# Performance work log

Measured on AMD Instinct MI355X. Metric: run time of the kernel, lower is better.

The kernel has to match this reference:

```python
import jax, jax.numpy as jnp
import numpy as np

D_MODEL = 1024
NUM_HEADS = 16
D_K = D_MODEL // NUM_HEADS
D_FF = 4096
LN_EPS = 1e-5


def layernorm(x, gamma, beta):
    mu = jnp.mean(x, axis=-1, keepdims=True)
    var = jnp.mean(jnp.square(x - mu), axis=-1, keepdims=True)
    return (x - mu) * jax.lax.rsqrt(var + LN_EPS) * gamma + beta


def setup_inputs() -> dict:
    key = jax.random.key(0)
    ks = jax.random.split(key, 16)
    s = 1.0 / np.sqrt(D_MODEL)
    sf = 1.0 / np.sqrt(D_FF)
    inp = {
        "x": jax.random.normal(ks[0], (2, 2048, D_MODEL), dtype=jnp.float32),
        # attention sublayer LN
        "ln1_g": jnp.ones((D_MODEL,), jnp.float32),
        "ln1_b": jnp.zeros((D_MODEL,), jnp.float32),
        # QKV / output projections, stored as [in, out]
        "Wq": jax.random.uniform(ks[1], (D_MODEL, D_MODEL), jnp.float32, -s, s),
        "bq": jax.random.uniform(ks[2], (D_MODEL,), jnp.float32, -s, s),
        "Wk": jax.random.uniform(ks[3], (D_MODEL, D_MODEL), jnp.float32, -s, s),
        "bk": jax.random.uniform(ks[4], (D_MODEL,), jnp.float32, -s, s),
        "Wv": jax.random.uniform(ks[5], (D_MODEL, D_MODEL), jnp.float32, -s, s),
        "bv": jax.random.uniform(ks[6], (D_MODEL,), jnp.float32, -s, s),
        "Wo": jax.random.uniform(ks[7], (D_MODEL, D_MODEL), jnp.float32, -s, s),
        "bo": jax.random.uniform(ks[8], (D_MODEL,), jnp.float32, -s, s),
        # FFN sublayer LN
        "ln2_g": jnp.ones((D_MODEL,), jnp.float32),
        "ln2_b": jnp.zeros((D_MODEL,), jnp.float32),
        "W1": jax.random.uniform(ks[9], (D_MODEL, D_FF), jnp.float32, -s, s),
        "b1": jax.random.uniform(ks[10], (D_FF,), jnp.float32, -s, s),
        "W2": jax.random.uniform(ks[11], (D_FF, D_MODEL), jnp.float32, -sf, sf),
        "b2": jax.random.uniform(ks[12], (D_MODEL,), jnp.float32, -sf, sf),
    }
    return inp


def block_fwd(x, ln1_g, ln1_b, Wq, bq, Wk, bk, Wv, bv, Wo, bo,
              ln2_g, ln2_b, W1, b1, W2, b2):
    B, S, D = x.shape
    # --- attention sublayer (pre-LN + residual) ---
    h = layernorm(x, ln1_g, ln1_b)
    q = (h @ Wq + bq).reshape(B, S, NUM_HEADS, D_K)
    k = (h @ Wk + bk).reshape(B, S, NUM_HEADS, D_K)
    v = (h @ Wv + bv).reshape(B, S, NUM_HEADS, D_K)
    scale = 1.0 / np.sqrt(D_K)  # == sqrt(d_k)/d_k in source
    attn = jnp.einsum("bqhd,bkhd->bhqk", q, k) * scale  # [B,H,S,S]
    causal = jnp.arange(S)[:, None] >= jnp.arange(S)[None, :]
    attn = jnp.where(causal, attn, -jnp.inf)
    score = jax.nn.softmax(attn, axis=-1)
    o = jnp.einsum("bhqk,bkhd->bqhd", score, v).reshape(B, S, D)
    x = x + (o @ Wo + bo)
    # --- FFN sublayer (pre-LN + residual) ---
    h = layernorm(x, ln2_g, ln2_b)
    h = jax.nn.gelu(h @ W1 + b1, approximate=False)  # torch nn.GELU = exact erf
    return x + (h @ W2 + b2)


def reference(x, ln1_g, ln1_b, Wq, bq, Wk, bk, Wv, bv, Wo, bo,
              ln2_g, ln2_b, W1, b1, W2, b2):
    return block_fwd(x, ln1_g, ln1_b, Wq, bq, Wk, bk, Wv, bv, Wo, bo,
                     ln2_g, ln2_b, W1, b1, W2, b2)
```

## Files before the change

### kernel.cpp

```cpp
#include <hip/hip_runtime.h>
#include <hip/hip_bf16.h>
#include <hip/hip_fp8.h>
#include <math.h>

typedef unsigned short u16;
typedef unsigned char u8;
typedef unsigned int u32;
typedef long i64;
typedef __bf16 bf16x8 __attribute__((ext_vector_type(8)));
typedef float f32x4 __attribute__((ext_vector_type(4)));

#define MFMA16(a, b, c) __builtin_amdgcn_mfma_f32_16x16x32_bf16(a, b, c, 0, 0, 0)
#define MFMA8(a, b, c) __builtin_amdgcn_mfma_f32_16x16x32_fp8_fp8(a, b, c, 0, 0, 0)

__device__ __forceinline__ u16 f2b(float f) {
    __bf16 h = (__bf16)f;
    return __builtin_bit_cast(u16, h);
}

__device__ __forceinline__ u8 f2f8(float f) {
    __hip_fp8_e4m3 h(f);
    return h.__x;
}

__device__ __forceinline__ void gld16(const void* g, void* l) {
    __builtin_amdgcn_global_load_lds(
        (const __attribute__((address_space(1))) unsigned int*)g,
        (__attribute__((address_space(3))) unsigned int*)l, 16, 0, 0);
}

__global__ __launch_bounds__(256) void transpose_all(
    const float* __restrict__ Wq, const float* __restrict__ Wk,
    const float* __restrict__ Wv, const float* __restrict__ Wo,
    const float* __restrict__ W1, const float* __restrict__ W2, u16* __restrict__ wqkvT,
    u16* __restrict__ woT, u16* __restrict__ w1T, u8* __restrict__ w2T8) {
    __shared__ float tile[32][33];
    int t = blockIdx.x;
    const float* in;
    u16* out = nullptr;
    int R, C;
    bool isf8 = false;
    if (t < 3072) {
        int m = t >> 10;
        t &= 1023;
        in = m == 0 ? Wq : (m == 1 ? Wk : Wv);
        out = wqkvT + m * 1048576;
        R = 1024; C = 1024;
    } else if (t < 4096) {
        t -= 3072; in = Wo; out = woT; R = 1024; C = 1024;
    } else if (t < 8192) {
        t -= 4096; in = W1; out = w1T; R = 1024; C = 4096;
    } else {
        t -= 8192; in = W2; R = 4096; C = 1024; isf8 = true;
    }
    int tilesX = C >> 5;
    int c0 = (t % tilesX) * 32, r0 = (t / tilesX) * 32;
    int tx = threadIdx.x, ty = threadIdx.y;
#pragma unroll
    for (int i = 0; i < 4; i++)
        tile[ty + i * 8][tx] = in[(size_t)(r0 + ty + i * 8) * C + c0 + tx];
    __syncthreads();
    if (isf8) {
#pragma unroll
        for (int i = 0; i < 4; i++)
            w2T8[(size_t)(c0 + ty + i * 8) * R + r0 + tx] = f2f8(tile[tx][ty + i * 8] * 64.0f);
    } else {
#pragma unroll
        for (int i = 0; i < 4; i++)
            out[(size_t)(c0 + ty + i * 8) * R + r0 + tx] = f2b(tile[tx][ty + i * 8]);
    }
}

__global__ __launch_bounds__(256) void ln_kernel(const float* __restrict__ x,
                                                 const float* __restrict__ g,
                                                 const float* __restrict__ b,
                                                 u16* __restrict__ out) {
    int row = blockIdx.x;
    int tid = threadIdx.x;
    const float* xr = x + (size_t)row * 1024;
    float4 v = ((const float4*)xr)[tid];
    float s = v.x + v.y + v.z + v.w;
    float s2 = v.x * v.x + v.y * v.y + v.z * v.z + v.w * v.w;
#pragma unroll
    for (int off = 32; off > 0; off >>= 1) {
        s += __shfl_xor(s, off);
        s2 += __shfl_xor(s2, off);
    }
    __shared__ float ps[4], ps2[4];
    int wid = tid >> 6;
    if ((tid & 63) == 0) { ps[wid] = s; ps2[wid] = s2; }
    __syncthreads();
    s = ps[0] + ps[1] + ps[2] + ps[3];
    s2 = ps2[0] + ps2[1] + ps2[2] + ps2[3];
    float mu = s * (1.0f / 1024.0f);
    float var = s2 * (1.0f / 1024.0f) - mu * mu;
    float rs = rsqrtf(var + 1e-5f);
    int c = tid * 4;
    ushort4 o;
    o.x = f2b((v.x - mu) * rs * g[c + 0] + b[c + 0]);
    o.y = f2b((v.y - mu) * rs * g[c + 1] + b[c + 1]);
    o.z = f2b((v.z - mu) * rs * g[c + 2] + b[c + 2]);
    o.w = f2b((v.w - mu) * rs * g[c + 3] + b[c + 3]);
    ((ushort4*)(out + (size_t)row * 1024))[tid] = o;
}

__global__ __launch_bounds__(256) void vtrans_kernel(const u16* __restrict__ Vb,
                                                     u16* __restrict__ VbT) {
    __shared__ u16 t[64][66];
    const int tid = threadIdx.x;
    const int s0 = blockIdx.x * 64;
    const int bh = blockIdx.y;
    const u16* src = Vb + (size_t)bh * 2048 * 64;
    u16* dst = VbT + (size_t)bh * 64 * 2048;
#pragma unroll
    for (int p = 0; p < 2; p++) {
        int idx = p * 256 + tid;
        int r = idx >> 3, dc = (idx & 7) * 8;
        uint4 v = *(const uint4*)&src[(size_t)(s0 + r) * 64 + dc];
        const u16* pv = (const u16*)&v;
#pragma unroll
        for (int j = 0; j < 8; j++) t[r][dc + j] = pv[j];
    }
    __syncthreads();
    int d = tid >> 2, sc = (tid & 3) * 16;
    u16 buf[16];
#pragma unroll
    for (int m = 0; m < 16; m++) {
        int cp = sc + m;
        int blk = cp >> 5, c = cp & 31;
        int srcw = blk * 32 + (c >> 1) + (c & 1) * 16;
        buf[m] = t[srcw][d];
    }
    *(uint4*)&dst[(size_t)d * 2048 + s0 + sc] = *(uint4*)&buf[0];
    *(uint4*)&dst[(size_t)d * 2048 + s0 + sc + 8] = *(uint4*)&buf[8];
}

#define EPI_QKV 0
#define EPI_RESID 1
#define EPI_GELU 2

__device__ __forceinline__ void gemm_stage(const u16* __restrict__ A,
                                           const u16* __restrict__ BT,
                                           u16 (&Asb)[128][32], u16 (&Bsb)[128][32],
                                           int m0, int n0, int K, int k0, int sr, int sdc,
                                           int wb) {
    gld16(&A[(size_t)(m0 + sr) * K + k0 + sdc], &Asb[0][0] + wb);
    gld16(&A[(size_t)(m0 + 64 + sr) * K + k0 + sdc], &Asb[0][0] + 2048 + wb);
    gld16(&BT[(size_t)(n0 + sr) * K + k0 + sdc], &Bsb[0][0] + wb);
    gld16(&BT[(size_t)(n0 + 64 + sr) * K + k0 + sdc], &Bsb[0][0] + 2048 + wb);
}

__device__ __forceinline__ void gemm_compute(const u16 (&Asb)[128][32],
                                             const u16 (&Bsb)[128][32], f32x4 (&acc)[4][4],
                                             int wm, int wn, int quad, int c15) {
    bf16x8 af[4], bfr[4];
#pragma unroll
    for (int i = 0; i < 4; i++) af[i] = *(const bf16x8*)&Asb[wm + i * 16 + c15][quad * 8];
#pragma unroll
    for (int j = 0; j < 4; j++) bfr[j] = *(const bf16x8*)&Bsb[wn + j * 16 + c15][quad * 8];
#pragma unroll
    for (int i = 0; i < 4; i++)
#pragma unroll
        for (int j = 0; j < 4; j++) acc[i][j] = MFMA16(af[i], bfr[j], acc[i][j]);
}

template <int EPI>
__global__ __launch_bounds__(256) void gemm_kernel(const u16* __restrict__ A,
                                                   const u16* __restrict__ BT,
                                                   const float* __restrict__ bias0,
                                                   const float* __restrict__ bias1,
                                                   const float* __restrict__ bias2,
                                                   void* __restrict__ outp,
                                                   const float* __restrict__ resid,
                                                   int N, int K) {
    __shared__ __align__(16) u16 As0[128][32], Bs0[128][32];
    __shared__ __align__(16) u16 As1[128][32], Bs1[128][32];
    const int tid = threadIdx.x;
    const int m0 = blockIdx.y * 128, n0 = blockIdx.x * 128;
    const int w = tid >> 6, lid = tid & 63, quad = lid >> 4, c15 = lid & 15;
    const int wm = (w >> 1) * 64, wn = (w & 1) * 64;
    const int sr = tid >> 2, sdc = (tid & 3) * 8;
    const int wb = (tid & 192) * 8;

    f32x4 acc[4][4] = {};

    gemm_stage(A, BT, As0, Bs0, m0, n0, K, 0, sr, sdc, wb);
    const int KT = K >> 5;
    for (int kt = 0; kt < KT; kt += 2) {
        __syncthreads();
        gemm_stage(A, BT, As1, Bs1, m0, n0, K, (kt + 1) << 5, sr, sdc, wb);
        gemm_compute(As0, Bs0, acc, wm, wn, quad, c15);
        __syncthreads();
        if (kt + 2 < KT) gemm_stage(A, BT, As0, Bs0, m0, n0, K, (kt + 2) << 5, sr, sdc, wb);
        gemm_compute(As1, Bs1, acc, wm, wn, quad, c15);
    }

    const int which = n0 >> 10;
    const float* bias = (EPI == EPI_QKV) ? (which == 0 ? bias0 : (which == 1 ? bias1 : bias2))
                                         : bias0;
    u16* qkv_dst = (u16*)outp + (size_t)which * 4194304;

#pragma unroll
    for (int i = 0; i < 4; i++) {
#pragma unroll
        for (int j = 0; j < 4; j++) {
#pragma unroll
            for (int r = 0; r < 4; r++) {
                int gr = m0 + wm + i * 16 + quad * 4 + r;
                int gc = n0 + wn + j * 16 + c15;
                if (EPI == EPI_QKV) {
                    int lc = gc & 1023;
                    float v = acc[i][j][r] + bias[lc];
                    int bb = gr >> 11, ss = gr & 2047, hh = lc >> 6, dd = lc & 63;
                    qkv_dst[((size_t)((bb * 16 + hh) * 2048 + ss)) * 64 + dd] = f2b(v);
                } else if (EPI == EPI_RESID) {
                    float v = acc[i][j][r] + bias[gc];
                    ((float*)outp)[(size_t)gr * N + gc] = resid[(size_t)gr * N + gc] + v;
                } else {
                    float v = acc[i][j][r] + bias[gc];
                    float u = v * (0.79788456f + 0.03567741f * v * v);
                    float e = __expf(2.0f * u);
                    float th = 1.0f - 2.0f / (e + 1.0f);
                    ((u8*)outp)[(size_t)gr * N + gc] = f2f8(0.5f * v * (1.0f + th));
                }
            }
        }
    }
}

__device__ __forceinline__ void gemm8_stage(const u8* __restrict__ A,
                                            const u8* __restrict__ BT, u8 (&Asb)[128][32],
                                            u8 (&Bsb)[128][32], int m0, int n0, int K,
                                            int k0, int sr, int sdc, int wbB) {
    gld16(&A[(size_t)(m0 + sr) * K + k0 + sdc], &Asb[0][0] + wbB);
    gld16(&BT[(size_t)(n0 + sr) * K + k0 + sdc], &Bsb[0][0] + wbB);
}

__device__ __forceinline__ void gemm8_compute(const u8 (&Asb)[128][32],
                                              const u8 (&Bsb)[128][32], f32x4 (&acc)[4][4],
                                              int wm, int wn, int quad, int c15) {
    i64 af[4], bfr[4];
#pragma unroll
    for (int i = 0; i < 4; i++) af[i] = *(const i64*)&Asb[wm + i * 16 + c15][quad * 8];
#pragma unroll
    for (int j = 0; j < 4; j++) bfr[j] = *(const i64*)&Bsb[wn + j * 16 + c15][quad * 8];
#pragma unroll
    for (int i = 0; i < 4; i++)
#pragma unroll
        for (int j = 0; j < 4; j++) acc[i][j] = MFMA8(af[i], bfr[j], acc[i][j]);
}

__global__ __launch_bounds__(256) void gemm_fp8_kernel(const u8* __restrict__ A,
                                                       const u8* __restrict__ BT,
                                                       const float* __restrict__ bias,
                                                       float* __restrict__ outp,
                                                       const float* __restrict__ resid,
                                                       int N, int K) {
    __shared__ __align__(16) u8 As0[128][32], Bs0[128][32];
    __shared__ __align__(16) u8 As1[128][32], Bs1[128][32];
    const int tid = threadIdx.x;
    const int m0 = blockIdx.y * 128, n0 = blockIdx.x * 128;
    const int w = tid >> 6, lid = tid & 63, quad = lid >> 4, c15 = lid & 15;
    const int wm = (w >> 1) * 64, wn = (w & 1) * 64;
    const int sr = tid >> 1, sdc = (tid & 1) * 16;
    const int wbB = (tid & 192) * 16;

    f32x4 acc[4][4] = {};

    gemm8_stage(A, BT, As0, Bs0, m0, n0, K, 0, sr, sdc, wbB);
    const int KT = K >> 5;
    for (int kt = 0; kt < KT; kt += 2) {
        __syncthreads();
        gemm8_stage(A, BT, As1, Bs1, m0, n0, K, (kt + 1) << 5, sr, sdc, wbB);
        gemm8_compute(As0, Bs0, acc, wm, wn, quad, c15);
        __syncthreads();
        if (kt + 2 < KT) gemm8_stage(A, BT, As0, Bs0, m0, n0, K, (kt + 2) << 5, sr, sdc, wbB);
        gemm8_compute(As1, Bs1, acc, wm, wn, quad, c15);
    }

#pragma unroll
    for (int i = 0; i < 4; i++) {
#pragma unroll
        for (int j = 0; j < 4; j++) {
#pragma unroll
            for (int r = 0; r < 4; r++) {
                int gr = m0 + wm + i * 16 + quad * 4 + r;
                int gc = n0 + wn + j * 16 + c15;
                float v = acc[i][j][r] * (1.0f / 64.0f) + bias[gc];
                outp[(size_t)gr * N + gc] = resid[(size_t)gr * N + gc] + v;
            }
        }
    }
}

__device__ __forceinline__ void attn_step(const u16 (&KB)[2][64][32],
                                          const u16 (&VB)[2][64][32],
                                          u16 (&Psw)[2][32][40], const bf16x8 (&aq)[2][2],
                                          f32x4 (&o)[2][4], float (&lsum)[2][4], int kv0,
                                          int qr0, int quad, int c15) {
    if (kv0 > qr0 + 31) return;
    bf16x8 bk[4][2];
#pragma unroll
    for (int nf = 0; nf < 4; nf++)
#pragma unroll
        for (int kd = 0; kd < 2; kd++)
            bk[nf][kd] = *(const bf16x8*)&KB[kd][nf * 16 + c15][quad * 8];
    f32x4 sf[2][4];
#pragma unroll
    for (int qf = 0; qf < 2; qf++)
#pragma unroll
        for (int nf = 0; nf < 4; nf++) {
            f32x4 s = {};
            s = MFMA16(aq[qf][0], bk[nf][0], s);
            s = MFMA16(aq[qf][1], bk[nf][1], s);
            sf[qf][nf] = s;
        }
    const bool domask = (kv0 + 63 > qr0);
    if (domask) {
#pragma unroll
        for (int qf = 0; qf < 2; qf++)
#pragma unroll
            for (int r = 0; r < 4; r++) {
                int rowg = qr0 + qf * 16 + quad * 4 + r;
#pragma unroll
                for (int nf = 0; nf < 4; nf++) {
                    float p = (kv0 + nf * 16 + c15 <= rowg) ? __expf(sf[qf][nf][r] * 0.125f)
                                                            : 0.0f;
                    sf[qf][nf][r] = p;
                    lsum[qf][r] += p;
                }
            }
    } else {
#pragma unroll
        for (int qf = 0; qf < 2; qf++)
#pragma unroll
            for (int r = 0; r < 4; r++)
#pragma unroll
                for (int nf = 0; nf < 4; nf++) {
                    float p = __expf(sf[qf][nf][r] * 0.125f);
                    sf[qf][nf][r] = p;
                    lsum[qf][r] += p;
                }
    }
#pragma unroll
    for (int qf = 0; qf < 2; qf++)
#pragma unroll
        for (int ks = 0; ks < 2; ks++)
#pragma unroll
            for (int r = 0; r < 4; r++) {
                u32 pk = (u32)f2b(sf[qf][2 * ks][r]) | ((u32)f2b(sf[qf][2 * ks + 1][r]) << 16);
                *(u32*)&Psw[ks][qf * 16 + quad * 4 + r][2 * c15] = pk;
            }
    asm volatile("s_waitcnt lgkmcnt(0)" ::: "memory");
    bf16x8 ap[2][2];
#pragma unroll
    for (int qf = 0; qf < 2; qf++)
#pragma unroll
        for (int ks = 0; ks < 2; ks++)
            ap[qf][ks] = *(const bf16x8*)&Psw[ks][qf * 16 + c15][quad * 8];
#pragma unroll
    for (int df = 0; df < 4; df++) {
        bf16x8 bv0 = *(const bf16x8*)&VB[0][df * 16 + c15][quad * 8];
        bf16x8 bv1 = *(const bf16x8*)&VB[1][df * 16 + c15][quad * 8];
#pragma unroll
        for (int qf = 0; qf < 2; qf++) {
            o[qf][df] = MFMA16(ap[qf][0], bv0, o[qf][df]);
            o[qf][df] = MFMA16(ap[qf][1], bv1, o[qf][df]);
        }
    }
}

__global__ __launch_bounds__(256) void attn_kernel(const u16* __restrict__ Q,
                                                   const u16* __restrict__ Kb,
                                                   const u16* __restrict__ VbT,
                                                   u16* __restrict__ attO) {
    __shared__ __align__(16) u16 K0s[2][64][32], K1s[2][64][32];
    __shared__ __align__(16) u16 V0s[2][64][32], V1s[2][64][32];
    __shared__ __align__(16) u16 Ps[4][2][32][40];

    const int tid = threadIdx.x;
    const int bh = blockIdx.x;
    const int pj = blockIdx.y;
    const size_t base = (size_t)bh * 2048 * 64;
    const u16* Qp = Q + base;
    const u16* Kp = Kb + base;
    const u16* Vp = VbT + (size_t)bh * 64 * 2048;
    const int w = tid >> 6, lane = tid & 63, quad = lane >> 4, c15 = lane & 15;
    const int sr = tid >> 2, sdc = (tid & 3) * 8;
    const int wb = (tid & 192) * 8;
    const int bb = bh >> 4, hh = bh & 15;

#define ATTN_STAGE(KB, VB, kvo)                                                        \
    do {                                                                               \
        gld16(&Kp[(size_t)((kvo) + sr) * 64 + sdc], &KB[0][0][0] + wb);                \
        gld16(&Kp[(size_t)((kvo) + sr) * 64 + 32 + sdc], &KB[0][0][0] + 2048 + wb);    \
        gld16(&Vp[(size_t)sr * 2048 + (kvo) + sdc], &VB[0][0][0] + wb);                \
        gld16(&Vp[(size_t)sr * 2048 + (kvo) + 32 + sdc], &VB[0][0][0] + 2048 + wb);    \
    } while (0)

    auto run_tile = [&](int q0) {
        const int qr0 = q0 + w * 32;
        bf16x8 aq[2][2];
#pragma unroll
        for (int qf = 0; qf < 2; qf++)
#pragma unroll
            for (int ks = 0; ks < 2; ks++)
                aq[qf][ks] = *(const bf16x8*)&Qp[(size_t)(qr0 + qf * 16 + c15) * 64 +
                                                 ks * 32 + quad * 8];
        f32x4 o[2][4] = {};
        float lsum[2][4] = {};
        const int steps = (q0 >> 6) + 2;
        __syncthreads();
        ATTN_STAGE(K0s, V0s, 0);
        int s = 0;
        for (;;) {
            __syncthreads();
            if (s + 1 < steps) ATTN_STAGE(K1s, V1s, (s + 1) << 6);
            attn_step(K0s, V0s, Ps[w], aq, o, lsum, s << 6, qr0, quad, c15);
            if (++s >= steps) break;
            __syncthreads();
            if (s + 1 < steps) ATTN_STAGE(K0s, V0s, (s + 1) << 6);
            attn_step(K1s, V1s, Ps[w], aq, o, lsum, s << 6, qr0, quad, c15);
            if (++s >= steps) break;
        }
#pragma unroll
        for (int qf = 0; qf < 2; qf++)
#pragma unroll
            for (int r = 0; r < 4; r++) {
                float l = lsum[qf][r];
#pragma unroll
                for (int off = 1; off < 16; off <<= 1) l += __shfl_xor(l, off);
                float inv = 1.0f / l;
                int sg = qr0 + qf * 16 + quad * 4 + r;
                size_t rowoff = ((size_t)(bb * 2048 + sg)) * 1024 + hh * 64;
#pragma unroll
                for (int df = 0; df < 4; df++)
                    attO[rowoff + df * 16 + c15] = f2b(o[qf][df][r] * inv);
            }
    };
    run_tile((15 - pj) * 128);
    run_tile(pj * 128);
#undef ATTN_STAGE
}

extern "C" void kernel_launch(void* const* d_in, const int* in_sizes, int n_in,
                              void* d_out, int out_size, void* d_ws, size_t ws_size,
                              hipStream_t stream) {
    const float* x = (const float*)d_in[0];
    const float* ln1g = (const float*)d_in[1];
    const float* ln1b = (const float*)d_in[2];
    const float* Wq = (const float*)d_in[3];
    const float* bq = (const float*)d_in[4];
    const float* Wk = (const float*)d_in[5];
    const float* bk = (const float*)d_in[6];
    const float* Wv = (const float*)d_in[7];
    const float* bv = (const float*)d_in[8];
    const float* Wo = (const float*)d_in[9];
    const float* bo = (const float*)d_in[10];
    const float* ln2g = (const float*)d_in[11];
    const float* ln2b = (const float*)d_in[12];
    const float* W1 = (const float*)d_in[13];
    const float* b1 = (const float*)d_in[14];
    const float* W2 = (const float*)d_in[15];
    const float* b2 = (const float*)d_in[16];
    float* out = (float*)d_out;

    char* ws = (char*)d_ws;
    u16* wqkvT = (u16*)(ws + 0);
    u16* woT = (u16*)(ws + 6291456);
    u16* w1T = (u16*)(ws + 8388608);
    u8* w2T8 = (u8*)(ws + 16777216);
    u16* h = (u16*)(ws + 25165824);
    float* x1 = (float*)(ws + 33554432);
    u16* Qb = (u16*)(ws + 50331648);
    u16* Kb = (u16*)(ws + 58720256);
    u16* Vb = (u16*)(ws + 67108864);
    u16* VbT = (u16*)(ws + 75497472);
    u16* aO = Vb;
    u8* mid8 = (u8*)(ws + 50331648);

    transpose_all<<<12288, dim3(32, 8), 0, stream>>>(Wq, Wk, Wv, Wo, W1, W2, wqkvT, woT,
                                                     w1T, w2T8);

    ln_kernel<<<4096, 256, 0, stream>>>(x, ln1g, ln1b, h);

    gemm_kernel<EPI_QKV><<<dim3(24, 32), 256, 0, stream>>>(h, wqkvT, bq, bk, bv, Qb, nullptr,
                                                           3072, 1024);

    vtrans_kernel<<<dim3(32, 32), 256, 0, stream>>>(Vb, VbT);

    attn_kernel<<<dim3(32, 8), 256, 0, stream>>>(Qb, Kb, VbT, aO);

    gemm_kernel<EPI_RESID><<<dim3(8, 32), 256, 0, stream>>>(aO, woT, bo, nullptr, nullptr, x1,
                                                            x, 1024, 1024);

    ln_kernel<<<4096, 256, 0, stream>>>(x1, ln2g, ln2b, h);

    gemm_kernel<EPI_GELU><<<dim3(32, 32), 256, 0, stream>>>(h, w1T, b1, nullptr, nullptr, mid8,
                                                            nullptr, 4096, 1024);
    gemm_fp8_kernel<<<dim3(8, 32), 256, 0, stream>>>(mid8, w2T8, b2, out, x1, 1024, 4096);
}
```

Measured before the change: 366.0 us.

## Shrink GEMM/attention tiles for more blocks and use 64-wide K FP8 steps

The attention kernel now runs one 64-row query tile per block (1024 blocks instead of 256 with paired tiles), and each wave handles 16 query rows. The output-projection GEMM moves to a new 128x64 tile kernel, doubling its grid to 512 blocks. The FP8 down-projection also uses 128x64 tiles with a 64-byte K step, and W2T and the GELU output are written with a permuted K layout so each lane can load 16 contiguous bytes per fragment. The aim is better CU occupancy and load balance on a large GPU, at the cost of less data reuse per block and more redundant A-tile loads.

```diff
diff --git a/kernel.cpp b/kernel.cpp
--- a/kernel.cpp
+++ b/kernel.cpp
@@ -9,6 +9,7 @@
 typedef long i64;
 typedef __bf16 bf16x8 __attribute__((ext_vector_type(8)));
 typedef float f32x4 __attribute__((ext_vector_type(4)));
+typedef i64 i64x2 __attribute__((ext_vector_type(2)));
 
 #define MFMA16(a, b, c) __builtin_amdgcn_mfma_f32_16x16x32_bf16(a, b, c, 0, 0, 0)
 #define MFMA8(a, b, c) __builtin_amdgcn_mfma_f32_16x16x32_fp8_fp8(a, b, c, 0, 0, 0)
@@ -28,6 +29,7 @@
         (const __attribute__((address_space(1))) unsigned int*)g,
         (__attribute__((address_space(3))) unsigned int*)l, 16, 0, 0);
 }
+
 
 __global__ __launch_bounds__(256) void transpose_all(
     const float* __restrict__ Wq, const float* __restrict__ Wk,
@@ -61,9 +63,10 @@
         tile[ty + i * 8][tx] = in[(size_t)(r0 + ty + i * 8) * C + c0 + tx];
     __syncthreads();
     if (isf8) {
+        int pos = (r0 & ~63) + (tx >> 3) * 16 + ((r0 >> 5) & 1) * 8 + (tx & 7);
 #pragma unroll
         for (int i = 0; i < 4; i++)
-            w2T8[(size_t)(c0 + ty + i * 8) * R + r0 + tx] = f2f8(tile[tx][ty + i * 8] * 64.0f);
+            w2T8[(size_t)(c0 + ty + i * 8) * 4096 + pos] = f2f8(tile[tx][ty + i * 8] * 64.0f);
     } else {
 #pragma unroll
         for (int i = 0; i < 4; i++)
@@ -221,33 +224,73 @@
                     float u = v * (0.79788456f + 0.03567741f * v * v);
                     float e = __expf(2.0f * u);
                     float th = 1.0f - 2.0f / (e + 1.0f);
-                    ((u8*)outp)[(size_t)gr * N + gc] = f2f8(0.5f * v * (1.0f + th));
+                    int g = gc & 63;
+                    int pos = (gc & ~63) + ((g >> 3) & 3) * 16 + (g >> 5) * 8 + (g & 7);
+                    ((u8*)outp)[(size_t)gr * N + pos] = f2f8(0.5f * v * (1.0f + th));
                 }
             }
         }
     }
 }
 
-__device__ __forceinline__ void gemm8_stage(const u8* __restrict__ A,
-                                            const u8* __restrict__ BT, u8 (&Asb)[128][32],
-                                            u8 (&Bsb)[128][32], int m0, int n0, int K,
-                                            int k0, int sr, int sdc, int wbB) {
-    gld16(&A[(size_t)(m0 + sr) * K + k0 + sdc], &Asb[0][0] + wbB);
-    gld16(&BT[(size_t)(n0 + sr) * K + k0 + sdc], &Bsb[0][0] + wbB);
-}
-
-__device__ __forceinline__ void gemm8_compute(const u8 (&Asb)[128][32],
-                                              const u8 (&Bsb)[128][32], f32x4 (&acc)[4][4],
-                                              int wm, int wn, int quad, int c15) {
-    i64 af[4], bfr[4];
-#pragma unroll
-    for (int i = 0; i < 4; i++) af[i] = *(const i64*)&Asb[wm + i * 16 + c15][quad * 8];
-#pragma unroll
-    for (int j = 0; j < 4; j++) bfr[j] = *(const i64*)&Bsb[wn + j * 16 + c15][quad * 8];
-#pragma unroll
-    for (int i = 0; i < 4; i++)
-#pragma unroll
-        for (int j = 0; j < 4; j++) acc[i][j] = MFMA8(af[i], bfr[j], acc[i][j]);
+__global__ __launch_bounds__(256) void gemm64_kernel(const u16* __restrict__ A,
+                                                     const u16* __restrict__ BT,
+                                                     const float* __restrict__ bias,
+                                                     float* __restrict__ outp,
+                                                     const float* __restrict__ resid,
+                                                     int N, int K) {
+    __shared__ __align__(16) u16 As0[128][32], Bs0[64][32];
+    __shared__ __align__(16) u16 As1[128][32], Bs1[64][32];
+    const int tid = threadIdx.x;
+    const int m0 = blockIdx.y * 128, n0 = blockIdx.x * 64;
+    const int w = tid >> 6, lid = tid & 63, quad = lid >> 4, c15 = lid & 15;
+    const int wm = (w >> 1) * 64, wn = (w & 1) * 32;
+    const int sr = tid >> 2, sdc = (tid & 3) * 8;
+    const int wb = (tid & 192) * 8;
+
+    f32x4 acc[4][2] = {};
+
+    auto stage = [&](u16 (&Asb)[128][32], u16 (&Bsb)[64][32], int k0) {
+        gld16(&A[(size_t)(m0 + sr) * K + k0 + sdc], &Asb[0][0] + wb);
+        gld16(&A[(size_t)(m0 + 64 + sr) * K + k0 + sdc], &Asb[0][0] + 2048 + wb);
+        gld16(&BT[(size_t)(n0 + sr) * K + k0 + sdc], &Bsb[0][0] + wb);
+    };
+    auto compute = [&](const u16 (&Asb)[128][32], const u16 (&Bsb)[64][32]) {
+        bf16x8 af[4], bfr[2];
+#pragma unroll
+        for (int i = 0; i < 4; i++) af[i] = *(const bf16x8*)&Asb[wm + i * 16 + c15][quad * 8];
+#pragma unroll
+        for (int j = 0; j < 2; j++) bfr[j] = *(const bf16x8*)&Bsb[wn + j * 16 + c15][quad * 8];
+#pragma unroll
+        for (int i = 0; i < 4; i++)
+#pragma unroll
+            for (int j = 0; j < 2; j++) acc[i][j] = MFMA16(af[i], bfr[j], acc[i][j]);
+    };
+
+    stage(As0, Bs0, 0);
+    const int KT = K >> 5;
+    for (int kt = 0; kt < KT; kt += 2) {
+        __syncthreads();
+        stage(As1, Bs1, (kt + 1) << 5);
+        compute(As0, Bs0);
+        __syncthreads();
+        if (kt + 2 < KT) stage(As0, Bs0, (kt + 2) << 5);
+        compute(As1, Bs1);
+    }
+
+#pragma unroll
+    for (int i = 0; i < 4; i++) {
+#pragma unroll
+        for (int j = 0; j < 2; j++) {
+#pragma unroll
+            for (int r = 0; r < 4; r++) {
+                int gr = m0 + wm + i * 16 + quad * 4 + r;
+                int gc = n0 + wn + j * 16 + c15;
+                float v = acc[i][j][r] + bias[gc];
+                outp[(size_t)gr * N + gc] = resid[(size_t)gr * N + gc] + v;
+            }
+        }
+    }
 }
 
 __global__ __launch_bounds__(256) void gemm_fp8_kernel(const u8* __restrict__ A,
@@ -256,32 +299,54 @@
                                                        float* __restrict__ outp,
                                                        const float* __restrict__ resid,
                                                        int N, int K) {
-    __shared__ __align__(16) u8 As0[128][32], Bs0[128][32];
-    __shared__ __align__(16) u8 As1[128][32], Bs1[128][32];
+    __shared__ __align__(16) u8 As0[128][64], Bs0[64][64];
+    __shared__ __align__(16) u8 As1[128][64], Bs1[64][64];
     const int tid = threadIdx.x;
-    const int m0 = blockIdx.y * 128, n0 = blockIdx.x * 128;
+    const int m0 = blockIdx.y * 128, n0 = blockIdx.x * 64;
     const int w = tid >> 6, lid = tid & 63, quad = lid >> 4, c15 = lid & 15;
-    const int wm = (w >> 1) * 64, wn = (w & 1) * 64;
-    const int sr = tid >> 1, sdc = (tid & 1) * 16;
+    const int wm = (w >> 1) * 64, wn = (w & 1) * 32;
+    const int sr = tid >> 2, sdc = (tid & 3) * 16;
     const int wbB = (tid & 192) * 16;
 
-    f32x4 acc[4][4] = {};
-
-    gemm8_stage(A, BT, As0, Bs0, m0, n0, K, 0, sr, sdc, wbB);
-    const int KT = K >> 5;
+    f32x4 acc[4][2] = {};
+
+    auto stage = [&](u8 (&Asb)[128][64], u8 (&Bsb)[64][64], int k0) {
+        gld16(&A[(size_t)(m0 + sr) * K + k0 + sdc], &Asb[0][0] + wbB);
+        gld16(&A[(size_t)(m0 + 64 + sr) * K + k0 + sdc], &Asb[0][0] + 4096 + wbB);
+        gld16(&BT[(size_t)(n0 + sr) * K + k0 + sdc], &Bsb[0][0] + wbB);
+    };
+    auto compute = [&](const u8 (&Asb)[128][64], const u8 (&Bsb)[64][64]) {
+        i64x2 af[4], bfr[2];
+#pragma unroll
+        for (int i = 0; i < 4; i++)
+            af[i] = *(const i64x2*)&Asb[wm + i * 16 + c15][quad * 16];
+#pragma unroll
+        for (int j = 0; j < 2; j++)
+            bfr[j] = *(const i64x2*)&Bsb[wn + j * 16 + c15][quad * 16];
+#pragma unroll
+        for (int s = 0; s < 2; s++)
+#pragma unroll
+            for (int i = 0; i < 4; i++)
+#pragma unroll
+                for (int j = 0; j < 2; j++)
+                    acc[i][j] = MFMA8(af[i][s], bfr[j][s], acc[i][j]);
+    };
+
+    stage(As0, Bs0, 0);
+    const int KT = K >> 6;
     for (int kt = 0; kt < KT; kt += 2) {
         __syncthreads();
-        gemm8_stage(A, BT, As1, Bs1, m0, n0, K, (kt + 1) << 5, sr, sdc, wbB);
-        gemm8_compute(As0, Bs0, acc, wm, wn, quad, c15);
-        __syncthreads();
-        if (kt + 2 < KT) gemm8_stage(A, BT, As0, Bs0, m0, n0, K, (kt + 2) << 5, sr, sdc, wbB);
-        gemm8_compute(As1, Bs1, acc, wm, wn, quad, c15);
+        stage(As1, Bs1, (kt + 1) << 6);
+        compute(As0, Bs0);
+        __syncthreads();
+        if (kt + 2 < KT) stage(As0, Bs0, (kt + 2) << 6);
+        compute(As1, Bs1);
     }
 
 #pragma unroll
     for (int i = 0; i < 4; i++) {
 #pragma unroll
-        for (int j = 0; j < 4; j++) {
+        for (int j = 0; j < 2; j++) {
 #pragma unroll
             for (int r = 0; r < 4; r++) {
                 int gr = m0 + wm + i * 16 + quad * 4 + r;
@@ -295,78 +360,62 @@
 
 __device__ __forceinline__ void attn_step(const u16 (&KB)[2][64][32],
                                           const u16 (&VB)[2][64][32],
-                                          u16 (&Psw)[2][32][40], const bf16x8 (&aq)[2][2],
-                                          f32x4 (&o)[2][4], float (&lsum)[2][4], int kv0,
+                                          u16 (&Psw)[2][16][48], const bf16x8 (&aq)[2],
+                                          f32x4 (&o)[4], float (&lsum)[4], int kv0,
                                           int qr0, int quad, int c15) {
-    if (kv0 > qr0 + 31) return;
     bf16x8 bk[4][2];
 #pragma unroll
     for (int nf = 0; nf < 4; nf++)
 #pragma unroll
         for (int kd = 0; kd < 2; kd++)
             bk[nf][kd] = *(const bf16x8*)&KB[kd][nf * 16 + c15][quad * 8];
-    f32x4 sf[2][4];
-#pragma unroll
-    for (int qf = 0; qf < 2; qf++)
-#pragma unroll
-        for (int nf = 0; nf < 4; nf++) {
-            f32x4 s = {};
-            s = MFMA16(aq[qf][0], bk[nf][0], s);
-            s = MFMA16(aq[qf][1], bk[nf][1], s);
-            sf[qf][nf] = s;
-        }
+    f32x4 sf[4];
+#pragma unroll
+    for (int nf = 0; nf < 4; nf++) {
+        f32x4 s = {};
+        s = MFMA16(aq[0], bk[nf][0], s);
+        s = MFMA16(aq[1], bk[nf][1], s);
+        sf[nf] = s;
+    }
     const bool domask = (kv0 + 63 > qr0);
     if (domask) {
 #pragma unroll
-        for (int qf = 0; qf < 2; qf++)
-#pragma unroll
-            for (int r = 0; r < 4; r++) {
-                int rowg = qr0 + qf * 16 + quad * 4 + r;
-#pragma unroll
-                for (int nf = 0; nf < 4; nf++) {
-                    float p = (kv0 + nf * 16 + c15 <= rowg) ? __expf(sf[qf][nf][r] * 0.125f)
-                                                            : 0.0f;
-                    sf[qf][nf][r] = p;
-                    lsum[qf][r] += p;
-                }
+        for (int r = 0; r < 4; r++) {
+            int rowg = qr0 + quad * 4 + r;
+#pragma unroll
+            for (int nf = 0; nf < 4; nf++) {
+                float p = (kv0 + nf * 16 + c15 <= rowg) ? __expf(sf[nf][r] * 0.125f) : 0.0f;
+                sf[nf][r] = p;
+                lsum[r] += p;
             }
+        }
     } else {
 #pragma unroll
-        for (int qf = 0; qf < 2; qf++)
-#pragma unroll
-            for (int r = 0; r < 4; r++)
-#pragma unroll
-                for (int nf = 0; nf < 4; nf++) {
-                    float p = __expf(sf[qf][nf][r] * 0.125f);
-                    sf[qf][nf][r] = p;
-                    lsum[qf][r] += p;
-                }
-    }
-#pragma unroll
-    for (int qf = 0; qf < 2; qf++)
-#pragma unroll
-        for (int ks = 0; ks < 2; ks++)
-#pragma unroll
-            for (int r = 0; r < 4; r++) {
-                u32 pk = (u32)f2b(sf[qf][2 * ks][r]) | ((u32)f2b(sf[qf][2 * ks + 1][r]) << 16);
-                *(u32*)&Psw[ks][qf * 16 + quad * 4 + r][2 * c15] = pk;
+        for (int r = 0; r < 4; r++)
+#pragma unroll
+            for (int nf = 0; nf < 4; nf++) {
+                float p = __expf(sf[nf][r] * 0.125f);
+                sf[nf][r] = p;
+                lsum[r] += p;
             }
+    }
+#pragma unroll
+    for (int ks = 0; ks < 2; ks++)
+#pragma unroll
+        for (int r = 0; r < 4; r++) {
+            u32 pk = (u32)f2b(sf[2 * ks][r]) | ((u32)f2b(sf[2 * ks + 1][r]) << 16);
+            *(u32*)&Psw[ks][quad * 4 + r][2 * c15] = pk;
+        }
     asm volatile("s_waitcnt lgkmcnt(0)" ::: "memory");
-    bf16x8 ap[2][2];
-#pragma unroll
-    for (int qf = 0; qf < 2; qf++)
-#pragma unroll
-        for (int ks = 0; ks < 2; ks++)
-            ap[qf][ks] = *(const bf16x8*)&Psw[ks][qf * 16 + c15][quad * 8];
+    bf16x8 ap[2];
+#pragma unroll
+    for (int ks = 0; ks < 2; ks++) ap[ks] = *(const bf16x8*)&Psw[ks][c15][quad * 8];
 #pragma unroll
     for (int df = 0; df < 4; df++) {
         bf16x8 bv0 = *(const bf16x8*)&VB[0][df * 16 + c15][quad * 8];
         bf16x8 bv1 = *(const bf16x8*)&VB[1][df * 16 + c15][quad * 8];
-#pragma unroll
-        for (int qf = 0; qf < 2; qf++) {
-            o[qf][df] = MFMA16(ap[qf][0], bv0, o[qf][df]);
-            o[qf][df] = MFMA16(ap[qf][1], bv1, o[qf][df]);
-        }
+        o[df] = MFMA16(ap[0], bv0, o[df]);
+        o[df] = MFMA16(ap[1], bv1, o[df]);
     }
 }
 
@@ -374,72 +423,59 @@
                                                    const u16* __restrict__ Kb,
                                                    const u16* __restrict__ VbT,
                                                    u16* __restrict__ attO) {
-    __shared__ __align__(16) u16 K0s[2][64][32], K1s[2][64][32];
-    __shared__ __align__(16) u16 V0s[2][64][32], V1s[2][64][32];
-    __shared__ __align__(16) u16 Ps[4][2][32][40];
+    __shared__ __align__(16) u16 Ks[2][2][64][32];
+    __shared__ __align__(16) u16 Vs[2][2][64][32];
+    __shared__ __align__(16) u16 Ps[4][2][16][48];
 
     const int tid = threadIdx.x;
     const int bh = blockIdx.x;
-    const int pj = blockIdx.y;
+    const int qt = 31 - blockIdx.y;
+    const int q0 = qt * 64;
     const size_t base = (size_t)bh * 2048 * 64;
     const u16* Qp = Q + base;
     const u16* Kp = Kb + base;
     const u16* Vp = VbT + (size_t)bh * 64 * 2048;
     const int w = tid >> 6, lane = tid & 63, quad = lane >> 4, c15 = lane & 15;
+    const int qr0 = q0 + w * 16;
     const int sr = tid >> 2, sdc = (tid & 3) * 8;
     const int wb = (tid & 192) * 8;
     const int bb = bh >> 4, hh = bh & 15;
 
-#define ATTN_STAGE(KB, VB, kvo)                                                        \
-    do {                                                                               \
-        gld16(&Kp[(size_t)((kvo) + sr) * 64 + sdc], &KB[0][0][0] + wb);                \
-        gld16(&Kp[(size_t)((kvo) + sr) * 64 + 32 + sdc], &KB[0][0][0] + 2048 + wb);    \
-        gld16(&Vp[(size_t)sr * 2048 + (kvo) + sdc], &VB[0][0][0] + wb);                \
-        gld16(&Vp[(size_t)sr * 2048 + (kvo) + 32 + sdc], &VB[0][0][0] + 2048 + wb);    \
+#define ATTN_STAGE(bi, kvo)                                                             \
+    do {                                                                                \
+        gld16(&Kp[(size_t)((kvo) + sr) * 64 + sdc], &Ks[bi][0][0][0] + wb);             \
+        gld16(&Kp[(size_t)((kvo) + sr) * 64 + 32 + sdc], &Ks[bi][0][0][0] + 2048 + wb); \
+        gld16(&Vp[(size_t)sr * 2048 + (kvo) + sdc], &Vs[bi][0][0][0] + wb);             \
+        gld16(&Vp[(size_t)sr * 2048 + (kvo) + 32 + sdc], &Vs[bi][0][0][0] + 2048 + wb); \
     } while (0)
 
-    auto run_tile = [&](int q0) {
-        const int qr0 = q0 + w * 32;
-        bf16x8 aq[2][2];
-#pragma unroll
-        for (int qf = 0; qf < 2; qf++)
-#pragma unroll
-            for (int ks = 0; ks < 2; ks++)
-                aq[qf][ks] = *(const bf16x8*)&Qp[(size_t)(qr0 + qf * 16 + c15) * 64 +
-                                                 ks * 32 + quad * 8];
-        f32x4 o[2][4] = {};
-        float lsum[2][4] = {};
-        const int steps = (q0 >> 6) + 2;
-        __syncthreads();
-        ATTN_STAGE(K0s, V0s, 0);
-        int s = 0;
-        for (;;) {
-            __syncthreads();
-            if (s + 1 < steps) ATTN_STAGE(K1s, V1s, (s + 1) << 6);
-            attn_step(K0s, V0s, Ps[w], aq, o, lsum, s << 6, qr0, quad, c15);
-            if (++s >= steps) break;
-            __syncthreads();
-            if (s + 1 < steps) ATTN_STAGE(K0s, V0s, (s + 1) << 6);
-            attn_step(K1s, V1s, Ps[w], aq, o, lsum, s << 6, qr0, quad, c15);
-            if (++s >= steps) break;
-        }
-#pragma unroll
-        for (int qf = 0; qf < 2; qf++)
-#pragma unroll
-            for (int r = 0; r < 4; r++) {
-                float l = lsum[qf][r];
-#pragma unroll
-                for (int off = 1; off < 16; off <<= 1) l += __shfl_xor(l, off);
-                float inv = 1.0f / l;
-                int sg = qr0 + qf * 16 + quad * 4 + r;
-                size_t rowoff = ((size_t)(bb * 2048 + sg)) * 1024 + hh * 64;
-#pragma unroll
-                for (int df = 0; df < 4; df++)
-                    attO[rowoff + df * 16 + c15] = f2b(o[qf][df][r] * inv);
-            }
-    };
-    run_tile((15 - pj) * 128);
-    run_tile(pj * 128);
+    bf16x8 aq[2];
+#pragma unroll
+    for (int ks = 0; ks < 2; ks++)
+        aq[ks] = *(const bf16x8*)&Qp[(size_t)(qr0 + c15) * 64 + ks * 32 + quad * 8];
+
+    f32x4 o[4] = {};
+    float lsum[4] = {};
+    const int steps = qt + 1;
+
+    ATTN_STAGE(0, 0);
+    for (int s = 0; s < steps; s++) {
+        __syncthreads();
+        if (s + 1 < steps) ATTN_STAGE((s + 1) & 1, (s + 1) << 6);
+        attn_step(Ks[s & 1], Vs[s & 1], Ps[w], aq, o, lsum, s << 6, qr0, quad, c15);
+    }
+
+#pragma unroll
+    for (int r = 0; r < 4; r++) {
+        float l = lsum[r];
+#pragma unroll
+        for (int off = 1; off < 16; off <<= 1) l += __shfl_xor(l, off);
+        float inv = 1.0f / l;
+        int sg = qr0 + quad * 4 + r;
+        size_t rowoff = ((size_t)(bb * 2048 + sg)) * 1024 + hh * 64;
+#pragma unroll
+        for (int df = 0; df < 4; df++) attO[rowoff + df * 16 + c15] = f2b(o[df][r] * inv);
+    }
 #undef ATTN_STAGE
 }
 
@@ -489,14 +525,13 @@
 
     vtrans_kernel<<<dim3(32, 32), 256, 0, stream>>>(Vb, VbT);
 
-    attn_kernel<<<dim3(32, 8), 256, 0, stream>>>(Qb, Kb, VbT, aO);
-
-    gemm_kernel<EPI_RESID><<<dim3(8, 32), 256, 0, stream>>>(aO, woT, bo, nullptr, nullptr, x1,
-                                                            x, 1024, 1024);
+    attn_kernel<<<dim3(32, 32), 256, 0, stream>>>(Qb, Kb, VbT, aO);
+
+    gemm64_kernel<<<dim3(16, 32), 256, 0, stream>>>(aO, woT, bo, x1, x, 1024, 1024);
 
     ln_kernel<<<4096, 256, 0, stream>>>(x1, ln2g, ln2b, h);
 
     gemm_kernel<EPI_GELU><<<dim3(32, 32), 256, 0, stream>>>(h, w1T, b1, nullptr, nullptr, mid8,
                                                             nullptr, 4096, 1024);
-    gemm_fp8_kernel<<<dim3(8, 32), 256, 0, stream>>>(mid8, w2T8, b2, out, x1, 1024, 4096);
-}
+    gemm_fp8_kernel<<<dim3(16, 32), 256, 0, stream>>>(mid8, w2T8, b2, out, x1, 1024, 4096);
+}
```

Result: faster. 323.1 us (-11.7%).
